# Optimization experiments

Measured on AMD Instinct MI355X. Metric: run time of the kernel, lower is better.

The kernel has to match this reference:

```python
import jax, jax.numpy as jnp
import numpy as np

B, N, D, H = 2, 2048, 768, 12
HD = D // H  # 64


def apply_rotary_embed(x, thetas):
    # x: (..., N, HD), thetas: (N, HD) broadcast over leading dims
    x1, x2 = jnp.split(x, 2, axis=-1)
    x_rot = jnp.concatenate([-x2, x1], axis=-1)
    return x * jnp.cos(thetas) + x_rot * jnp.sin(thetas)


def setup_inputs() -> dict:
    key = jax.random.key(0)
    ks = jax.random.split(key, 5)
    s = 0.02
    return {
        "x": jax.random.normal(ks[0], (B, N, D), dtype=jnp.float32),
        "pos_embed": jax.random.normal(ks[1], (N, HD), dtype=jnp.float32),
        "Wqkv": jax.random.normal(ks[2], (3 * D, D), dtype=jnp.float32) * s,
        "Wproj": jax.random.normal(ks[3], (D, D), dtype=jnp.float32) * s,
        "bproj": jnp.zeros((D,), dtype=jnp.float32),
    }


def reference(x, pos_embed, Wqkv, Wproj, bproj):
    Bb, Nn, Dd = x.shape
    # fused QKV projection (torch Linear: x @ W.T), no bias
    qkv = jnp.einsum('bnd,ed->bne', x, Wqkv)                 # (B, N, 3D)
    qkv = qkv.reshape(Bb, Nn, 3, H, HD).transpose(2, 0, 3, 1, 4)  # (3, B, H, N, HD)
    q, k, v = qkv[0], qkv[1], qkv[2]
    # rotary embedding on q and k
    q = apply_rotary_embed(q, pos_embed)
    k = apply_rotary_embed(k, pos_embed)
    # scaled dot-product attention (non-causal, no mask, no dropout)
    scale = 1.0 / jnp.sqrt(jnp.asarray(HD, dtype=x.dtype))
    scores = jnp.einsum('bhqd,bhkd->bhqk', q, k) * scale     # (B, H, N, N)
    attn = jax.nn.softmax(scores, axis=-1)
    out = jnp.einsum('bhqk,bhkd->bhqd', attn, v)             # (B, H, N, HD)
    out = out.transpose(0, 2, 1, 3).reshape(Bb, Nn, Dd)      # (B, N, D)
    # output projection (with bias)
    return jnp.einsum('bnd,ed->bne', out, Wproj) + bproj
```

## Files before the change

### kernel.cpp

```cpp
#include <hip/hip_runtime.h>
#include <stdint.h>

typedef __attribute__((ext_vector_type(8))) short short8;
typedef __attribute__((ext_vector_type(4))) float floatx4;
typedef __attribute__((ext_vector_type(16))) float floatx16;

#define BB 2
#define NN 2048
#define DD 768
#define HH 12
#define HDD 64
#define MM (BB*NN)

__device__ __forceinline__ unsigned short f2bf(float f) {
  unsigned int u = __builtin_bit_cast(unsigned int, f);
  u += 0x7fffu + ((u >> 16) & 1u);
  return (unsigned short)(u >> 16);
}
__device__ __forceinline__ float bf2f(unsigned short u) {
  unsigned int v = ((unsigned int)u) << 16;
  return __builtin_bit_cast(float, v);
}

__device__ __forceinline__ void gld16(const unsigned short* g, unsigned short* l) {
  __builtin_amdgcn_global_load_lds(
      (const __attribute__((address_space(1))) void*)g,
      (__attribute__((address_space(3))) void*)l, 16, 0, 0);
}

__global__ void cvt4_kernel(const float* __restrict__ src,
                            unsigned short* __restrict__ dst, int n4) {
  int i = blockIdx.x * blockDim.x + threadIdx.x;
  if (i >= n4) return;
  float4 v = reinterpret_cast<const float4*>(src)[i];
  unsigned int lo = (unsigned int)f2bf(v.x) | ((unsigned int)f2bf(v.y) << 16);
  unsigned int hi = (unsigned int)f2bf(v.z) | ((unsigned int)f2bf(v.w) << 16);
  reinterpret_cast<uint2*>(dst)[i] = make_uint2(lo, hi);
}

template<int MODE, int MT>
__global__ __launch_bounds__(256) void gemm_bt(
    const unsigned short* __restrict__ A,
    const unsigned short* __restrict__ Bt,
    void* __restrict__ Cout, const float* __restrict__ bias,
    int Nn, int K)
{
  constexpr int MTC = MT / 32;
  __shared__ __align__(16) unsigned short as_[MT*32];
  __shared__ __align__(16) unsigned short bs_[128*32];
  const int t = threadIdx.x;
  const int w = t >> 6, lane = t & 63;
  const int quad = lane >> 4, l16 = lane & 15;
  const int wm = (w >> 1) * (MT/2), wn = (w & 1) * 64;
  const int m0 = blockIdx.y * MT, n0 = blockIdx.x * 128;

  const floatx4 fz = {0.f, 0.f, 0.f, 0.f};
  floatx4 acc[MTC][4];
#pragma unroll
  for (int mt = 0; mt < MTC; mt++)
#pragma unroll
    for (int nt = 0; nt < 4; nt++) acc[mt][nt] = fz;

  for (int k0 = 0; k0 < K; k0 += 32) {
    __syncthreads();
#pragma unroll
    for (int i = 0; i < MT/64; i++) {
      int c = t + i * 256;
      gld16(&A[(size_t)(m0 + (c >> 2))*K + k0 + (c & 3)*8], &as_[c*8]);
    }
#pragma unroll
    for (int i = 0; i < 2; i++) {
      int c = t + i * 256;
      gld16(&Bt[(size_t)(n0 + (c >> 2))*K + k0 + (c & 3)*8], &bs_[c*8]);
    }
    __syncthreads();
    short8 af[MTC], bfr[4];
#pragma unroll
    for (int mt = 0; mt < MTC; mt++)
      af[mt] = *reinterpret_cast<const short8*>(&as_[(wm + mt*16 + l16)*32 + quad*8]);
#pragma unroll
    for (int nt = 0; nt < 4; nt++)
      bfr[nt] = *reinterpret_cast<const short8*>(&bs_[(wn + nt*16 + l16)*32 + quad*8]);
#pragma unroll
    for (int mt = 0; mt < MTC; mt++)
#pragma unroll
      for (int nt = 0; nt < 4; nt++)
        acc[mt][nt] = __builtin_amdgcn_mfma_f32_16x16x32_bf16(af[mt], bfr[nt], acc[mt][nt], 0, 0, 0);
  }
#pragma unroll
  for (int mt = 0; mt < MTC; mt++)
#pragma unroll
    for (int nt = 0; nt < 4; nt++)
#pragma unroll
      for (int r = 0; r < 4; r++) {
        int gm = m0 + wm + mt*16 + quad*4 + r;
        int gn = n0 + wn + nt*16 + l16;
        float v = acc[mt][nt][r];
        if (MODE == 0)
          reinterpret_cast<unsigned short*>(Cout)[(size_t)gm * Nn + gn] = f2bf(v);
        else
          reinterpret_cast<float*>(Cout)[(size_t)gm * Nn + gn] = v + bias[gn];
      }
}

__global__ __launch_bounds__(256) void rope_relayout(
    const unsigned short* __restrict__ qkv, const float* __restrict__ pos,
    unsigned short* __restrict__ qb, unsigned short* __restrict__ kb,
    unsigned short* __restrict__ vb)
{
  __shared__ __align__(16) unsigned short vt_l[64*72];
  const int n0 = blockIdx.x * 64;
  const int bh = blockIdx.y;
  const int b = bh / HH, hh = bh % HH;
  const int t = threadIdx.x;
  const int nl = t >> 2, j = t & 3;
  const int n = n0 + nl;
  const size_t qrow = (size_t)(b*NN + n) * (3*DD) + hh*HDD;

  union U8 { int4 v; unsigned short u[8]; };
  U8 qlo, qhi, klo, khi, vlo, vhi, qolo, qohi, kolo, kohi;
  qlo.v = *(const int4*)&qkv[qrow + j*8];
  qhi.v = *(const int4*)&qkv[qrow + 32 + j*8];
  klo.v = *(const int4*)&qkv[qrow + DD + j*8];
  khi.v = *(const int4*)&qkv[qrow + DD + 32 + j*8];
  vlo.v = *(const int4*)&qkv[qrow + 2*DD + j*8];
  vhi.v = *(const int4*)&qkv[qrow + 2*DD + 32 + j*8];
  float4 tl0 = *(const float4*)&pos[n*HDD + j*8];
  float4 tl1 = *(const float4*)&pos[n*HDD + j*8 + 4];
  float4 th0 = *(const float4*)&pos[n*HDD + 32 + j*8];
  float4 th1 = *(const float4*)&pos[n*HDD + 32 + j*8 + 4];
  float tl[8] = {tl0.x,tl0.y,tl0.z,tl0.w,tl1.x,tl1.y,tl1.z,tl1.w};
  float th[8] = {th0.x,th0.y,th0.z,th0.w,th1.x,th1.y,th1.z,th1.w};
#pragma unroll
  for (int e = 0; e < 8; e++) {
    float sl, cl, sh, ch;
    __sincosf(tl[e], &sl, &cl);
    __sincosf(th[e], &sh, &ch);
    float q1 = bf2f(qlo.u[e]), q2 = bf2f(qhi.u[e]);
    float k1 = bf2f(klo.u[e]), k2 = bf2f(khi.u[e]);
    qolo.u[e] = f2bf((q1*cl - q2*sl) * 0.125f);
    qohi.u[e] = f2bf((q2*ch + q1*sh) * 0.125f);
    kolo.u[e] = f2bf(k1*cl - k2*sl);
    kohi.u[e] = f2bf(k2*ch + k1*sh);
  }
  size_t obase = ((size_t)bh*NN + n) * HDD;
  *(int4*)&qb[obase + j*8] = qolo.v;
  *(int4*)&qb[obase + 32 + j*8] = qohi.v;
  *(int4*)&kb[obase + ((j       ^ (n & 7)) * 8)] = kolo.v;
  *(int4*)&kb[obase + (((j + 4) ^ (n & 7)) * 8)] = kohi.v;
#pragma unroll
  for (int e = 0; e < 8; e++) {
    vt_l[(j*8 + e)*72 + nl]      = vlo.u[e];
    vt_l[(j*8 + 32 + e)*72 + nl] = vhi.u[e];
  }
  __syncthreads();
  int hd = t >> 2;
#pragma unroll
  for (int u = 0; u < 2; u++) {
    int cc = (t & 3) + u * 4;
    int4 vv = *(const int4*)&vt_l[hd*72 + cc*8];
    int cg = ((n0 & 64) >> 3) + cc;
    int cswz = cg ^ (hd & 7);
    *(int4*)&vb[((size_t)bh*HDD + hd)*NN + (size_t)(n0 & ~127) + cswz*8] = vv;
  }
}

__global__ __launch_bounds__(128) void flash_attn(
    const unsigned short* __restrict__ qb, const unsigned short* __restrict__ kb,
    const unsigned short* __restrict__ vb, unsigned short* __restrict__ ob)
{
  __shared__ __align__(16) unsigned short ks[128*64];
  __shared__ __align__(16) unsigned short vt[64*128];
  __shared__ __align__(16) unsigned short ps[64*128];
  __shared__ __align__(16) float lsd[64];
  const int qt = blockIdx.x, bh = blockIdx.y;
  const int b = bh / HH, hh = bh % HH;
  const int t = threadIdx.x;
  const int w = t >> 6, lane = t & 63;
  const int l32 = lane & 31, hf = lane >> 5;
  const int q0 = qt * 64;
  const size_t kbase = (size_t)bh * (NN*HDD);

  short8 qf[4];
  {
    const unsigned short* qp = &qb[((size_t)bh*NN + q0 + w*32 + l32)*HDD + hf*8];
#pragma unroll
    for (int s = 0; s < 4; s++) qf[s] = *(const short8*)&qp[s*16];
  }
  floatx16 fz16;
#pragma unroll
  for (int z = 0; z < 16; z++) fz16[z] = 0.f;
  floatx16 oacc[2];
  oacc[0] = fz16; oacc[1] = fz16;
  float lrow = 0.f;

  for (int kt = 0; kt < NN/128; kt++) {
    __syncthreads();
#pragma unroll
    for (int i = 0; i < 8; i++) {
      int c = i*128 + t;
      gld16(&kb[kbase + (size_t)kt*8192 + c*8], &ks[c*8]);
      gld16(&vb[kbase + (size_t)(c >> 4)*NN + kt*128 + (c & 15)*8], &vt[c*8]);
    }
    __syncthreads();

    floatx16 sv[4];
#pragma unroll
    for (int t2 = 0; t2 < 4; t2++) {
      floatx16 acc;
#pragma unroll
      for (int z = 0; z < 16; z++) acc[z] = 0.f;
      int row = t2*32 + l32;
#pragma unroll
      for (int s = 0; s < 4; s++) {
        int cd = (2*s + hf) ^ (l32 & 7);
        short8 kf = *(const short8*)&ks[row*64 + cd*8];
        acc = __builtin_amdgcn_mfma_f32_32x32x16_bf16(kf, qf[s], acc, 0, 0, 0);
      }
      sv[t2] = acc;
    }
    float rs = 0.f;
    unsigned short* pr = &ps[(w*32 + l32)*128];
#pragma unroll
    for (int t2 = 0; t2 < 4; t2++) {
      float pv_[16];
#pragma unroll
      for (int r = 0; r < 16; r++) { pv_[r] = __expf(sv[t2][r]); rs += pv_[r]; }
#pragma unroll
      for (int g = 0; g < 4; g++) {
        unsigned int x0 = __builtin_bit_cast(unsigned int, pv_[4*g+0]);
        unsigned int x1 = __builtin_bit_cast(unsigned int, pv_[4*g+1]);
        unsigned int x2 = __builtin_bit_cast(unsigned int, pv_[4*g+2]);
        unsigned int x3 = __builtin_bit_cast(unsigned int, pv_[4*g+3]);
        unsigned int lo = __builtin_amdgcn_perm(x1, x0, 0x07060302u);
        unsigned int hi = __builtin_amdgcn_perm(x3, x2, 0x07060302u);
        int slot = (t2*4 + g) ^ (l32 & 7);
        *(uint2*)&pr[slot*8 + hf*4] = make_uint2(lo, hi);
      }
    }
    rs += __shfl_xor(rs, 32);
    lrow += rs;
#pragma unroll
    for (int s2 = 0; s2 < 8; s2++) {
      int ca = (s2*2 + hf) ^ (l32 & 7);
      short8 pf = *(const short8*)&pr[ca*8];
#pragma unroll
      for (int ht = 0; ht < 2; ht++) {
        int hd = ht*32 + l32;
        short8 vf = *(const short8*)&vt[hd*128 + ca*8];
        oacc[ht] = __builtin_amdgcn_mfma_f32_32x32x16_bf16(pf, vf, oacc[ht], 0, 0, 0);
      }
    }
  }
  if (hf == 0) lsd[w*32 + l32] = lrow;
#pragma unroll
  for (int g = 0; g < 4; g++) {
    floatx4 l4 = *(const floatx4*)&lsd[w*32 + g*8 + hf*4];
#pragma unroll
    for (int e = 0; e < 4; e++) {
      float inv = 1.f / l4[e];
      int qrow = q0 + w*32 + g*8 + hf*4 + e;
#pragma unroll
      for (int ht = 0; ht < 2; ht++)
        ob[((size_t)(b*NN + qrow))*DD + hh*HDD + ht*32 + l32] = f2bf(oacc[ht][4*g+e] * inv);
    }
  }
}

extern "C" void kernel_launch(void* const* d_in, const int* in_sizes, int n_in,
                              void* d_out, int out_size, void* d_ws, size_t ws_size,
                              hipStream_t stream)
{
  const float* x     = (const float*)d_in[0];
  const float* pos   = (const float*)d_in[1];
  const float* Wqkv  = (const float*)d_in[2];
  const float* Wproj = (const float*)d_in[3];
  const float* bproj = (const float*)d_in[4];

  unsigned short* p = (unsigned short*)d_ws;
  unsigned short* xb     = p; p += (size_t)MM*DD;
  unsigned short* wqkvb  = p; p += (size_t)3*DD*DD;
  unsigned short* wprojb = p; p += (size_t)DD*DD;
  unsigned short* qkvrm  = p; p += (size_t)MM*3*DD;
  unsigned short* qb     = p; p += (size_t)BB*HH*NN*HDD;
  unsigned short* kb     = p; p += (size_t)BB*HH*NN*HDD;
  unsigned short* vb     = p; p += (size_t)BB*HH*NN*HDD;
  unsigned short* ob     = qkvrm;

  cvt4_kernel<<<(MM*DD/4 + 255)/256, 256, 0, stream>>>(x, xb, MM*DD/4);
  cvt4_kernel<<<(3*DD*DD/4 + 255)/256, 256, 0, stream>>>(Wqkv, wqkvb, 3*DD*DD/4);
  cvt4_kernel<<<(DD*DD/4 + 255)/256, 256, 0, stream>>>(Wproj, wprojb, DD*DD/4);

  gemm_bt<0,64><<<dim3(3*DD/128, MM/64), 256, 0, stream>>>(xb, wqkvb, qkvrm, nullptr, 3*DD, DD);
  rope_relayout<<<dim3(NN/64, BB*HH), 256, 0, stream>>>(qkvrm, pos, qb, kb, vb);
  flash_attn<<<dim3(NN/64, BB*HH), 128, 0, stream>>>(qb, kb, vb, ob);
  gemm_bt<1,64><<<dim3(DD/128, MM/64), 256, 0, stream>>>(ob, wprojb, (float*)d_out, bproj, DD, DD);
}
```

Before: 188.0 us.

## Split attention key tile across wave pairs and merge conversion kernels

The flash attention block grows from 2 to 4 waves. Each pair of waves shares a 32-row query group and splits every 128-key tile in half. Partial output accumulators and row sums are combined through shared memory at the end. The three fp32-to-bf16 conversion launches are also merged into one kernel to cut launch overhead. The aim is more waves per block to hide latency and fewer serial MFMAs per wave, at the cost of an extra reduction through LDS and more synchronisation.

```diff
diff --git a/kernel.cpp b/kernel.cpp
--- a/kernel.cpp
+++ b/kernel.cpp
@@ -28,14 +28,20 @@
       (__attribute__((address_space(3))) void*)l, 16, 0, 0);
 }
 
-__global__ void cvt4_kernel(const float* __restrict__ src,
-                            unsigned short* __restrict__ dst, int n4) {
+__global__ void cvt_all(const float* __restrict__ x, const float* __restrict__ wq,
+                        const float* __restrict__ wp, unsigned short* __restrict__ xb,
+                        unsigned short* __restrict__ wqb, unsigned short* __restrict__ wpb) {
+  const int n1 = MM*DD/4, n2 = 3*DD*DD/4, n3 = DD*DD/4;
   int i = blockIdx.x * blockDim.x + threadIdx.x;
-  if (i >= n4) return;
-  float4 v = reinterpret_cast<const float4*>(src)[i];
+  const float* s; unsigned short* d; int j;
+  if (i < n1)            { s = x;  d = xb;  j = i; }
+  else if (i < n1+n2)    { s = wq; d = wqb; j = i - n1; }
+  else if (i < n1+n2+n3) { s = wp; d = wpb; j = i - n1 - n2; }
+  else return;
+  float4 v = reinterpret_cast<const float4*>(s)[j];
   unsigned int lo = (unsigned int)f2bf(v.x) | ((unsigned int)f2bf(v.y) << 16);
   unsigned int hi = (unsigned int)f2bf(v.z) | ((unsigned int)f2bf(v.w) << 16);
-  reinterpret_cast<uint2*>(dst)[i] = make_uint2(lo, hi);
+  reinterpret_cast<uint2*>(d)[j] = make_uint2(lo, hi);
 }
 
 template<int MODE, int MT>
@@ -165,25 +171,27 @@
   }
 }
 
-__global__ __launch_bounds__(128) void flash_attn(
+__global__ __launch_bounds__(256) void flash_attn(
     const unsigned short* __restrict__ qb, const unsigned short* __restrict__ kb,
     const unsigned short* __restrict__ vb, unsigned short* __restrict__ ob)
 {
   __shared__ __align__(16) unsigned short ks[128*64];
   __shared__ __align__(16) unsigned short vt[64*128];
   __shared__ __align__(16) unsigned short ps[64*128];
-  __shared__ __align__(16) float lsd[64];
+  __shared__ __align__(16) float lsd[128];
   const int qt = blockIdx.x, bh = blockIdx.y;
   const int b = bh / HH, hh = bh % HH;
   const int t = threadIdx.x;
   const int w = t >> 6, lane = t & 63;
   const int l32 = lane & 31, hf = lane >> 5;
+  const int gq = w >> 1;
+  const int kh = w & 1;
   const int q0 = qt * 64;
   const size_t kbase = (size_t)bh * (NN*HDD);
 
   short8 qf[4];
   {
-    const unsigned short* qp = &qb[((size_t)bh*NN + q0 + w*32 + l32)*HDD + hf*8];
+    const unsigned short* qp = &qb[((size_t)bh*NN + q0 + gq*32 + l32)*HDD + hf*8];
 #pragma unroll
     for (int s = 0; s < 4; s++) qf[s] = *(const short8*)&qp[s*16];
   }
@@ -197,19 +205,20 @@
   for (int kt = 0; kt < NN/128; kt++) {
     __syncthreads();
 #pragma unroll
-    for (int i = 0; i < 8; i++) {
-      int c = i*128 + t;
+    for (int i = 0; i < 4; i++) {
+      int c = i*256 + t;
       gld16(&kb[kbase + (size_t)kt*8192 + c*8], &ks[c*8]);
       gld16(&vb[kbase + (size_t)(c >> 4)*NN + kt*128 + (c & 15)*8], &vt[c*8]);
     }
     __syncthreads();
 
-    floatx16 sv[4];
-#pragma unroll
-    for (int t2 = 0; t2 < 4; t2++) {
+    floatx16 sv[2];
+#pragma unroll
+    for (int tt = 0; tt < 2; tt++) {
       floatx16 acc;
 #pragma unroll
       for (int z = 0; z < 16; z++) acc[z] = 0.f;
+      int t2 = kh*2 + tt;
       int row = t2*32 + l32;
 #pragma unroll
       for (int s = 0; s < 4; s++) {
@@ -217,15 +226,16 @@
         short8 kf = *(const short8*)&ks[row*64 + cd*8];
         acc = __builtin_amdgcn_mfma_f32_32x32x16_bf16(kf, qf[s], acc, 0, 0, 0);
       }
-      sv[t2] = acc;
+      sv[tt] = acc;
     }
     float rs = 0.f;
-    unsigned short* pr = &ps[(w*32 + l32)*128];
-#pragma unroll
-    for (int t2 = 0; t2 < 4; t2++) {
+    unsigned short* pr = &ps[(gq*32 + l32)*128];
+#pragma unroll
+    for (int tt = 0; tt < 2; tt++) {
+      int t2 = kh*2 + tt;
       float pv_[16];
 #pragma unroll
-      for (int r = 0; r < 16; r++) { pv_[r] = __expf(sv[t2][r]); rs += pv_[r]; }
+      for (int r = 0; r < 16; r++) { pv_[r] = __expf(sv[tt][r]); rs += pv_[r]; }
 #pragma unroll
       for (int g = 0; g < 4; g++) {
         unsigned int x0 = __builtin_bit_cast(unsigned int, pv_[4*g+0]);
@@ -241,7 +251,8 @@
     rs += __shfl_xor(rs, 32);
     lrow += rs;
 #pragma unroll
-    for (int s2 = 0; s2 < 8; s2++) {
+    for (int ss = 0; ss < 4; ss++) {
+      int s2 = kh*4 + ss;
       int ca = (s2*2 + hf) ^ (l32 & 7);
       short8 pf = *(const short8*)&pr[ca*8];
 #pragma unroll
@@ -252,18 +263,38 @@
       }
     }
   }
+  __syncthreads();
+  float* om = (float*)ps;
+  if (kh) {
+    float* base = om + gq*2048;
+#pragma unroll
+    for (int ht = 0; ht < 2; ht++)
+#pragma unroll
+      for (int g = 0; g < 4; g++)
+#pragma unroll
+        for (int e = 0; e < 4; e++) {
+          int ql = hf*4 + g*8 + e;
+          base[ql*64 + ht*32 + l32] = oacc[ht][4*g+e];
+        }
+  }
   if (hf == 0) lsd[w*32 + l32] = lrow;
-#pragma unroll
-  for (int g = 0; g < 4; g++) {
-    floatx4 l4 = *(const floatx4*)&lsd[w*32 + g*8 + hf*4];
-#pragma unroll
-    for (int e = 0; e < 4; e++) {
-      float inv = 1.f / l4[e];
-      int qrow = q0 + w*32 + g*8 + hf*4 + e;
-#pragma unroll
-      for (int ht = 0; ht < 2; ht++)
-        ob[((size_t)(b*NN + qrow))*DD + hh*HDD + ht*32 + l32] = f2bf(oacc[ht][4*g+e] * inv);
-    }
+  __syncthreads();
+  if (!kh) {
+    float* base = om + gq*2048;
+#pragma unroll
+    for (int g = 0; g < 4; g++)
+#pragma unroll
+      for (int e = 0; e < 4; e++) {
+        int ql = hf*4 + g*8 + e;
+        float l = lsd[gq*64 + ql] + lsd[gq*64 + 32 + ql];
+        float inv = 1.f / l;
+        int qrow = q0 + gq*32 + ql;
+#pragma unroll
+        for (int ht = 0; ht < 2; ht++) {
+          float v = oacc[ht][4*g+e] + base[ql*64 + ht*32 + l32];
+          ob[((size_t)(b*NN + qrow))*DD + hh*HDD + ht*32 + l32] = f2bf(v * inv);
+        }
+      }
   }
 }
 
@@ -287,12 +318,11 @@
   unsigned short* vb     = p; p += (size_t)BB*HH*NN*HDD;
   unsigned short* ob     = qkvrm;
 
-  cvt4_kernel<<<(MM*DD/4 + 255)/256, 256, 0, stream>>>(x, xb, MM*DD/4);
-  cvt4_kernel<<<(3*DD*DD/4 + 255)/256, 256, 0, stream>>>(Wqkv, wqkvb, 3*DD*DD/4);
-  cvt4_kernel<<<(DD*DD/4 + 255)/256, 256, 0, stream>>>(Wproj, wprojb, DD*DD/4);
+  const int ncvt = MM*DD/4 + 3*DD*DD/4 + DD*DD/4;
+  cvt_all<<<ncvt/256, 256, 0, stream>>>(x, Wqkv, Wproj, xb, wqkvb, wprojb);
 
   gemm_bt<0,64><<<dim3(3*DD/128, MM/64), 256, 0, stream>>>(xb, wqkvb, qkvrm, nullptr, 3*DD, DD);
   rope_relayout<<<dim3(NN/64, BB*HH), 256, 0, stream>>>(qkvrm, pos, qb, kb, vb);
-  flash_attn<<<dim3(NN/64, BB*HH), 128, 0, stream>>>(qb, kb, vb, ob);
+  flash_attn<<<dim3(NN/64, BB*HH), 256, 0, stream>>>(qb, kb, vb, ob);
   gemm_bt<1,64><<<dim3(DD/128, MM/64), 256, 0, stream>>>(ob, wprojb, (float*)d_out, bproj, DD, DD);
 }
```

Measured after the change: 175.5 us. 1.07x faster.
